# Kernel optimization log

Measured on AMD Instinct MI355X. Metric: run time of the kernel, lower is better.

The kernel has to match this reference:

```python
import jax, jax.numpy as jnp
import numpy as np

EPS = 1e-12  # torch F.normalize eps

def _l2norm(v, axis):
    n = jnp.sqrt(jnp.sum(v * v, axis=axis, keepdims=True))
    return v / jnp.maximum(n, EPS)

def setup_inputs() -> dict:
    key = jax.random.key(0)
    ks = jax.random.split(key, 5)
    B, N, C, K = 16, 512, 384, 64
    return {
        "x": jax.random.normal(ks[0], (B, N, C), dtype=jnp.float32),
        "centers": jax.random.normal(ks[1], (C, K), dtype=jnp.float32),
        "tran_ms": jax.random.normal(ks[2], (K, N, N), dtype=jnp.float32),
        "proj_w": jax.random.normal(ks[3], (C, C), dtype=jnp.float32) * 0.02,
        "proj_b": jax.random.normal(ks[4], (C,), dtype=jnp.float32) * 0.02,
    }

def reference(x, centers, tran_ms, proj_w, proj_b):
    # x: [B,N,C]
    q = x.mean(axis=1)                              # [B,C] mean-pooled query
    qn = _l2norm(q, axis=-1)                        # F.normalize(q, dim=-1)
    cn = _l2norm(centers, axis=0)                   # F.normalize(centers, dim=0)
    attn = jax.nn.softmax(qn @ cn, axis=-1)         # [B,K] cluster routing weights
    # combine transition matrices: equivalent to the (B,K,N,N) repeat/sum,
    # expressed as a single contraction producing [B,N,N]
    tm = jnp.einsum('bk,knm->bnm', attn, tran_ms)   # [B,N,N]
    y = jnp.einsum('bnm,bmc->bnc', tm, x)           # bmm
    out = y @ proj_w.T + proj_b                     # nn.Linear(dim, dim)
    return out
```

## Files before the change

### kernel.cpp

```cpp
#include <hip/hip_runtime.h>
#include <math.h>
#include <stdint.h>

#define B_  16
#define N_  512
#define C_  384
#define K_  64
#define NN_ (N_*N_)

typedef short bf16x8 __attribute__((ext_vector_type(8)));
typedef float f32x4  __attribute__((ext_vector_type(4)));

__device__ __forceinline__ unsigned short f2bf(float f) {
    union { float f; unsigned u; } v; v.f = f;
    unsigned r = v.u + 0x7FFF + ((v.u >> 16) & 1);
    return (unsigned short)(r >> 16);
}
__device__ __forceinline__ unsigned pack2(float a, float b) {
    return ((unsigned)f2bf(b) << 16) | f2bf(a);
}

__device__ __forceinline__ void gl_lds16(const void* g, void* l) {
    __builtin_amdgcn_global_load_lds(
        (const __attribute__((address_space(1))) unsigned*)g,
        (__attribute__((address_space(3))) unsigned*)l, 16, 0, 0);
}

__device__ __forceinline__ void fma4(float4& c, float s, const float4& v) {
    c.x = fmaf(s, v.x, c.x);
    c.y = fmaf(s, v.y, c.y);
    c.z = fmaf(s, v.z, c.z);
    c.w = fmaf(s, v.w, c.w);
}

__global__ __launch_bounds__(384) void mean_kernel(const float* __restrict__ x,
                                                   float* __restrict__ part,
                                                   unsigned short* __restrict__ xb) {
    const int b = blockIdx.y;
    const int s = blockIdx.x;
    const int c = threadIdx.x;
    const size_t base = ((size_t)(b * N_ + s * 16)) * C_ + c;
    const float* xp = x + base;
    unsigned short* xo = xb + base;
    float acc = 0.f;
#pragma unroll
    for (int i = 0; i < 16; ++i) {
        float v = xp[(size_t)i * C_];
        acc += v;
        xo[(size_t)i * C_] = f2bf(v);
    }
    part[((size_t)b * 32 + s) * C_ + c] = acc;
}

__global__ __launch_bounds__(384) void attn_kernel(const float* __restrict__ part,
                                                   const float* __restrict__ centers,
                                                   float* __restrict__ attn) {
    __shared__ float q_lds[C_];
    __shared__ float red[6];
    const int b = blockIdx.x;
    const int tid = threadIdx.x;

    const float* pb = part + (size_t)b * 32 * C_ + tid;
    float s = 0.f;
#pragma unroll
    for (int i = 0; i < 32; ++i) s += pb[(size_t)i * C_];
    q_lds[tid] = s;
    float p2 = s * s;
#pragma unroll
    for (int off = 32; off > 0; off >>= 1) p2 += __shfl_xor(p2, off);
    if ((tid & 63) == 0) red[tid >> 6] = p2;
    __syncthreads();

    if (tid < 64) {
        const int k = tid;
        const float qn2 = red[0] + red[1] + red[2] + red[3] + red[4] + red[5];
        const float qnorm = fmaxf(sqrtf(qn2), 1e-12f);

        float dot = 0.f, cn2 = 0.f;
        for (int c = 0; c < C_; ++c) {
            float sv = centers[c * K_ + k];
            float qc = q_lds[c];
            dot = fmaf(qc, sv, dot);
            cn2 = fmaf(sv, sv, cn2);
        }
        const float logit = dot / (qnorm * fmaxf(sqrtf(cn2), 1e-12f));

        float m = logit;
#pragma unroll
        for (int off = 32; off > 0; off >>= 1) m = fmaxf(m, __shfl_xor(m, off));
        const float e = expf(logit - m);
        float ssum = e;
#pragma unroll
        for (int off = 32; off > 0; off >>= 1) ssum += __shfl_xor(ssum, off);
        attn[b * K_ + k] = e / ssum;
    }
}

__global__ __launch_bounds__(256) void tm_kernel(const float* __restrict__ tran,
                                                 const float* __restrict__ attn,
                                                 unsigned short* __restrict__ tmb) {
    __shared__ float a_s[K_ * B_];
    const int tid = threadIdx.x;
    for (int i = tid; i < K_ * B_; i += 256)
        a_s[i] = attn[(i & 15) * K_ + (i >> 4)];
    __syncthreads();

    const size_t j = ((size_t)blockIdx.x * 256 + tid) * 4;
    float4 acc[B_];
#pragma unroll
    for (int b = 0; b < B_; ++b) acc[b] = make_float4(0.f, 0.f, 0.f, 0.f);

    for (int k = 0; k < K_; ++k) {
        const float4 t = *(const float4*)(tran + (size_t)k * NN_ + j);
        const float4* wp = (const float4*)(a_s + k * 16);
        const float4 w0 = wp[0], w1 = wp[1], w2 = wp[2], w3 = wp[3];
        fma4(acc[0],  w0.x, t); fma4(acc[1],  w0.y, t);
        fma4(acc[2],  w0.z, t); fma4(acc[3],  w0.w, t);
        fma4(acc[4],  w1.x, t); fma4(acc[5],  w1.y, t);
        fma4(acc[6],  w1.z, t); fma4(acc[7],  w1.w, t);
        fma4(acc[8],  w2.x, t); fma4(acc[9],  w2.y, t);
        fma4(acc[10], w2.z, t); fma4(acc[11], w2.w, t);
        fma4(acc[12], w3.x, t); fma4(acc[13], w3.y, t);
        fma4(acc[14], w3.z, t); fma4(acc[15], w3.w, t);
    }
#pragma unroll
    for (int b = 0; b < B_; ++b) {
        *(uint2*)(tmb + (size_t)b * NN_ + j) =
            make_uint2(pack2(acc[b].x, acc[b].y), pack2(acc[b].z, acc[b].w));
    }
}

__global__ __launch_bounds__(256) void xw_mfma(const unsigned short* __restrict__ Xb,
                                               const float* __restrict__ Wf,
                                               unsigned short* __restrict__ xwT) {
    __shared__ unsigned short As[64 * 64];
    __shared__ unsigned short Bs[64 * 64];
    __shared__ float T[4][32 * 35];

    const int tid  = threadIdx.x;
    const int row0 = blockIdx.x * 64;
    const int col0 = blockIdx.y * 64;
    const int lane = tid & 63;
    const int w    = tid >> 6;
    const int wm   = w & 1, wn = w >> 1;
    const int quad = lane >> 4, l15 = lane & 15;

    const int sm = tid >> 3;
    const int sc = tid & 7;

    f32x4 acc[2][2] = {};

    for (int k0 = 0; k0 < C_; k0 += 64) {
        float4 wv[2][2];
#pragma unroll
        for (int p = 0; p < 2; ++p) {
            const int m  = p * 32 + sm;
            const int gc = sc ^ (m & 7);
            const float* src = Wf + (size_t)(col0 + m) * C_ + k0 + gc * 8;
            wv[p][0] = *(const float4*)(src);
            wv[p][1] = *(const float4*)(src + 4);
        }
        __syncthreads();
#pragma unroll
        for (int p = 0; p < 2; ++p) {
            const int m  = p * 32 + sm;
            const int gc = sc ^ (m & 7);
            gl_lds16(Xb + (size_t)(row0 + m) * C_ + k0 + gc * 8,
                     As + (p * 256 + tid) * 8);
            const uint4 u = make_uint4(pack2(wv[p][0].x, wv[p][0].y),
                                       pack2(wv[p][0].z, wv[p][0].w),
                                       pack2(wv[p][1].x, wv[p][1].y),
                                       pack2(wv[p][1].z, wv[p][1].w));
            *(uint4*)(Bs + (p * 256 + tid) * 8) = u;
        }
        __syncthreads();
#pragma unroll
        for (int kk = 0; kk < 2; ++kk) {
            bf16x8 afr[2], bfr[2];
#pragma unroll
            for (int mt = 0; mt < 2; ++mt) {
                const int mr = wm * 32 + mt * 16 + l15;
                const int kc = (kk * 4 + quad) ^ (mr & 7);
                afr[mt] = *(const bf16x8*)(As + mr * 64 + kc * 8);
            }
#pragma unroll
            for (int nt = 0; nt < 2; ++nt) {
                const int nr = wn * 32 + nt * 16 + l15;
                const int kc = (kk * 4 + quad) ^ (nr & 7);
                bfr[nt] = *(const bf16x8*)(Bs + nr * 64 + kc * 8);
            }
#pragma unroll
            for (int mt = 0; mt < 2; ++mt)
#pragma unroll
                for (int nt = 0; nt < 2; ++nt)
                    acc[mt][nt] = __builtin_amdgcn_mfma_f32_16x16x32_bf16(
                        afr[mt], bfr[nt], acc[mt][nt], 0, 0, 0);
        }
    }

#pragma unroll
    for (int mt = 0; mt < 2; ++mt)
#pragma unroll
        for (int nt = 0; nt < 2; ++nt)
#pragma unroll
            for (int r = 0; r < 4; ++r)
                T[w][(mt * 16 + quad * 4 + r) * 35 + nt * 16 + l15] = acc[mt][nt][r];
    __syncthreads();

    const int rw = row0 + wm * 32;
    const int b  = rw >> 9;
    const int m0 = rw & 511;
    const int c0 = col0 + wn * 32;
    unsigned short* dst = xwT + (size_t)b * C_ * N_;
#pragma unroll
    for (int i = 0; i < 8; ++i) {
        const int cl = i * 4 + quad;
        const int ml = l15 * 2;
        const float v0 = T[w][(ml + 0) * 35 + cl];
        const float v1 = T[w][(ml + 1) * 35 + cl];
        *(unsigned*)(dst + (size_t)(c0 + cl) * N_ + m0 + ml) = pack2(v0, v1);
    }
}

__global__ __launch_bounds__(256) void out_mfma(const unsigned short* __restrict__ Ab,
                                                const unsigned short* __restrict__ Bt,
                                                const float* __restrict__ bias,
                                                float* __restrict__ out) {
    __shared__ unsigned short As[64 * 64];
    __shared__ unsigned short Bs[64 * 64];

    const int tid  = threadIdx.x;
    const int b    = blockIdx.z;
    const int row0 = blockIdx.x * 64;
    const int col0 = blockIdx.y * 64;
    const int lane = tid & 63;
    const int w    = tid >> 6;
    const int wm   = w & 1, wn = w >> 1;
    const int quad = lane >> 4, l15 = lane & 15;

    const unsigned short* Abase = Ab + (size_t)b * N_ * N_;
    const unsigned short* Bbase = Bt + (size_t)b * C_ * N_;

    const int sm = tid >> 3;
    const int sc = tid & 7;

    f32x4 acc[2][2] = {};

    for (int k0 = 0; k0 < N_; k0 += 64) {
        __syncthreads();
#pragma unroll
        for (int p = 0; p < 2; ++p) {
            const int m  = p * 32 + sm;
            const int gc = sc ^ (m & 7);
            gl_lds16(Abase + (size_t)(row0 + m) * N_ + k0 + gc * 8,
                     As + (p * 256 + tid) * 8);
            gl_lds16(Bbase + (size_t)(col0 + m) * N_ + k0 + gc * 8,
                     Bs + (p * 256 + tid) * 8);
        }
        __syncthreads();
#pragma unroll
        for (int kk = 0; kk < 2; ++kk) {
            bf16x8 afr[2], bfr[2];
#pragma unroll
            for (int mt = 0; mt < 2; ++mt) {
                const int mr = wm * 32 + mt * 16 + l15;
                const int kc = (kk * 4 + quad) ^ (mr & 7);
                afr[mt] = *(const bf16x8*)(As + mr * 64 + kc * 8);
            }
#pragma unroll
            for (int nt = 0; nt < 2; ++nt) {
                const int nr = wn * 32 + nt * 16 + l15;
                const int kc = (kk * 4 + quad) ^ (nr & 7);
                bfr[nt] = *(const bf16x8*)(Bs + nr * 64 + kc * 8);
            }
#pragma unroll
            for (int mt = 0; mt < 2; ++mt)
#pragma unroll
                for (int nt = 0; nt < 2; ++nt)
                    acc[mt][nt] = __builtin_amdgcn_mfma_f32_16x16x32_bf16(
                        afr[mt], bfr[nt], acc[mt][nt], 0, 0, 0);
        }
    }

#pragma unroll
    for (int nt = 0; nt < 2; ++nt) {
        const int c  = col0 + wn * 32 + nt * 16 + l15;
        const float bv = bias[c];
#pragma unroll
        for (int mt = 0; mt < 2; ++mt) {
            const int rbase = row0 + wm * 32 + mt * 16 + quad * 4;
#pragma unroll
            for (int r = 0; r < 4; ++r)
                out[((size_t)(b * N_ + rbase + r)) * C_ + c] = acc[mt][nt][r] + bv;
        }
    }
}

extern "C" void kernel_launch(void* const* d_in, const int* in_sizes, int n_in,
                              void* d_out, int out_size, void* d_ws, size_t ws_size,
                              hipStream_t stream) {
    const float* x       = (const float*)d_in[0];
    const float* centers = (const float*)d_in[1];
    const float* tran    = (const float*)d_in[2];
    const float* proj_w  = (const float*)d_in[3];
    const float* proj_b  = (const float*)d_in[4];
    float* out = (float*)d_out;

    float* ws   = (float*)d_ws;
    float* part = ws;
    float* attn = ws + 196608;
    unsigned short* tmb = (unsigned short*)(ws + 197632);
    unsigned short* xwT = tmb + (size_t)B_ * N_ * N_;
    unsigned short* xb  = xwT + (size_t)B_ * C_ * N_;

    mean_kernel<<<dim3(32, 16), 384, 0, stream>>>(x, part, xb);
    attn_kernel<<<16, 384, 0, stream>>>(part, centers, attn);
    tm_kernel<<<256, 256, 0, stream>>>(tran, attn, tmb);
    xw_mfma<<<dim3(128, 6), 256, 0, stream>>>(xb, proj_w, xwT);
    out_mfma<<<dim3(8, 6, 16), 256, 0, stream>>>(tmb, xwT, proj_b, out);
}
```

Before: 163.5 us.

## Merge tm combine and x·W projection into one concurrent launch

Fuses the transition-matrix combine kernel and the x·Wᵀ MFMA kernel into one launch of 1024 blocks. The first 256 blocks do the combine and the rest do the projection GEMM, so the two independent stages can run at the same time on the GPU. This removes one launch and the serialization gap between them. The combine loop is also unrolled by two so two tran loads are in flight per iteration. It reuses the As LDS buffer for the attn weights. In exchange, the combine blocks inherit the GEMM kernel's larger LDS footprint, which may lower occupancy.

```diff
diff --git a/kernel.cpp b/kernel.cpp
--- a/kernel.cpp
+++ b/kernel.cpp
@@ -96,50 +96,67 @@
     }
 }
 
-__global__ __launch_bounds__(256) void tm_kernel(const float* __restrict__ tran,
-                                                 const float* __restrict__ attn,
-                                                 unsigned short* __restrict__ tmb) {
-    __shared__ float a_s[K_ * B_];
-    const int tid = threadIdx.x;
-    for (int i = tid; i < K_ * B_; i += 256)
-        a_s[i] = attn[(i & 15) * K_ + (i >> 4)];
-    __syncthreads();
-
-    const size_t j = ((size_t)blockIdx.x * 256 + tid) * 4;
-    float4 acc[B_];
-#pragma unroll
-    for (int b = 0; b < B_; ++b) acc[b] = make_float4(0.f, 0.f, 0.f, 0.f);
-
-    for (int k = 0; k < K_; ++k) {
-        const float4 t = *(const float4*)(tran + (size_t)k * NN_ + j);
-        const float4* wp = (const float4*)(a_s + k * 16);
-        const float4 w0 = wp[0], w1 = wp[1], w2 = wp[2], w3 = wp[3];
-        fma4(acc[0],  w0.x, t); fma4(acc[1],  w0.y, t);
-        fma4(acc[2],  w0.z, t); fma4(acc[3],  w0.w, t);
-        fma4(acc[4],  w1.x, t); fma4(acc[5],  w1.y, t);
-        fma4(acc[6],  w1.z, t); fma4(acc[7],  w1.w, t);
-        fma4(acc[8],  w2.x, t); fma4(acc[9],  w2.y, t);
-        fma4(acc[10], w2.z, t); fma4(acc[11], w2.w, t);
-        fma4(acc[12], w3.x, t); fma4(acc[13], w3.y, t);
-        fma4(acc[14], w3.z, t); fma4(acc[15], w3.w, t);
-    }
-#pragma unroll
-    for (int b = 0; b < B_; ++b) {
-        *(uint2*)(tmb + (size_t)b * NN_ + j) =
-            make_uint2(pack2(acc[b].x, acc[b].y), pack2(acc[b].z, acc[b].w));
-    }
-}
-
-__global__ __launch_bounds__(256) void xw_mfma(const unsigned short* __restrict__ Xb,
-                                               const float* __restrict__ Wf,
-                                               unsigned short* __restrict__ xwT) {
+__global__ __launch_bounds__(256) void tmxw_kernel(const float* __restrict__ tran,
+                                                   const float* __restrict__ attn,
+                                                   unsigned short* __restrict__ tmb,
+                                                   const unsigned short* __restrict__ Xb,
+                                                   const float* __restrict__ Wf,
+                                                   unsigned short* __restrict__ xwT) {
     __shared__ unsigned short As[64 * 64];
     __shared__ unsigned short Bs[64 * 64];
     __shared__ float T[4][32 * 35];
 
-    const int tid  = threadIdx.x;
-    const int row0 = blockIdx.x * 64;
-    const int col0 = blockIdx.y * 64;
+    const int tid = threadIdx.x;
+
+    if (blockIdx.x < 256) {
+        float* a_s = (float*)As;
+        for (int i = tid; i < K_ * B_; i += 256)
+            a_s[i] = attn[(i & 15) * K_ + (i >> 4)];
+        __syncthreads();
+
+        const size_t j = ((size_t)blockIdx.x * 256 + tid) * 4;
+        float4 acc[B_];
+#pragma unroll
+        for (int b = 0; b < B_; ++b) acc[b] = make_float4(0.f, 0.f, 0.f, 0.f);
+
+        for (int k = 0; k < K_; k += 2) {
+            const float4 t0 = *(const float4*)(tran + (size_t)k * NN_ + j);
+            const float4 t1 = *(const float4*)(tran + (size_t)(k + 1) * NN_ + j);
+            {
+                const float4* wp = (const float4*)(a_s + k * 16);
+                const float4 w0 = wp[0], w1 = wp[1], w2 = wp[2], w3 = wp[3];
+                fma4(acc[0],  w0.x, t0); fma4(acc[1],  w0.y, t0);
+                fma4(acc[2],  w0.z, t0); fma4(acc[3],  w0.w, t0);
+                fma4(acc[4],  w1.x, t0); fma4(acc[5],  w1.y, t0);
+                fma4(acc[6],  w1.z, t0); fma4(acc[7],  w1.w, t0);
+                fma4(acc[8],  w2.x, t0); fma4(acc[9],  w2.y, t0);
+                fma4(acc[10], w2.z, t0); fma4(acc[11], w2.w, t0);
+                fma4(acc[12], w3.x, t0); fma4(acc[13], w3.y, t0);
+                fma4(acc[14], w3.z, t0); fma4(acc[15], w3.w, t0);
+            }
+            {
+                const float4* wp = (const float4*)(a_s + (k + 1) * 16);
+                const float4 w0 = wp[0], w1 = wp[1], w2 = wp[2], w3 = wp[3];
+                fma4(acc[0],  w0.x, t1); fma4(acc[1],  w0.y, t1);
+                fma4(acc[2],  w0.z, t1); fma4(acc[3],  w0.w, t1);
+                fma4(acc[4],  w1.x, t1); fma4(acc[5],  w1.y, t1);
+                fma4(acc[6],  w1.z, t1); fma4(acc[7],  w1.w, t1);
+                fma4(acc[8],  w2.x, t1); fma4(acc[9],  w2.y, t1);
+                fma4(acc[10], w2.z, t1); fma4(acc[11], w2.w, t1);
+                fma4(acc[12], w3.x, t1); fma4(acc[13], w3.y, t1);
+                fma4(acc[14], w3.z, t1); fma4(acc[15], w3.w, t1);
+            }
+        }
+#pragma unroll
+        for (int b = 0; b < B_; ++b)
+            *(uint2*)(tmb + (size_t)b * NN_ + j) =
+                make_uint2(pack2(acc[b].x, acc[b].y), pack2(acc[b].z, acc[b].w));
+        return;
+    }
+
+    const int bid  = blockIdx.x - 256;
+    const int row0 = (bid & 127) * 64;
+    const int col0 = (bid >> 7) * 64;
     const int lane = tid & 63;
     const int w    = tid >> 6;
     const int wm   = w & 1, wn = w >> 1;
@@ -167,11 +184,11 @@
             const int gc = sc ^ (m & 7);
             gl_lds16(Xb + (size_t)(row0 + m) * C_ + k0 + gc * 8,
                      As + (p * 256 + tid) * 8);
-            const uint4 u = make_uint4(pack2(wv[p][0].x, wv[p][0].y),
-                                       pack2(wv[p][0].z, wv[p][0].w),
-                                       pack2(wv[p][1].x, wv[p][1].y),
-                                       pack2(wv[p][1].z, wv[p][1].w));
-            *(uint4*)(Bs + (p * 256 + tid) * 8) = u;
+            *(uint4*)(Bs + (p * 256 + tid) * 8) =
+                make_uint4(pack2(wv[p][0].x, wv[p][0].y),
+                           pack2(wv[p][0].z, wv[p][0].w),
+                           pack2(wv[p][1].x, wv[p][1].y),
+                           pack2(wv[p][1].z, wv[p][1].w));
         }
         __syncthreads();
 #pragma unroll
@@ -315,7 +332,6 @@
 
     mean_kernel<<<dim3(32, 16), 384, 0, stream>>>(x, part, xb);
     attn_kernel<<<16, 384, 0, stream>>>(part, centers, attn);
-    tm_kernel<<<256, 256, 0, stream>>>(tran, attn, tmb);
-    xw_mfma<<<dim3(128, 6), 256, 0, stream>>>(xb, proj_w, xwT);
+    tmxw_kernel<<<1024, 256, 0, stream>>>(tran, attn, tmb, xb, proj_w, xwT);
     out_mfma<<<dim3(8, 6, 16), 256, 0, stream>>>(tmb, xwT, proj_b, out);
 }
```

Result: faster. 151.4 us (-7.4%).
